# Performance work log

Measured on AMD Instinct MI355X. Metric: run time of the kernel, lower is better.

Reference implementation:

```python
import jax, jax.numpy as jnp
import numpy as np

B, D_IN, D_OUT = 8192, 4096, 2048

def setup_inputs() -> dict:
    key = jax.random.key(0)
    k1, k2, k3 = jax.random.split(key, 3)
    inputs = jax.random.normal(k1, (B, D_IN), dtype=jnp.float32)
    # xavier-uniform kernel
    limit = float(np.sqrt(6.0 / (D_IN + D_OUT)))
    kernel = jax.random.uniform(k2, (D_IN, D_OUT), dtype=jnp.float32, minval=-limit, maxval=limit)
    bias = jnp.zeros((D_OUT,), dtype=jnp.float32)
    map_ = jax.random.bernoulli(k3, p=0.1, shape=(D_IN, D_OUT)).astype(jnp.float32)
    return {"inputs": inputs, "kernel": kernel, "bias": bias, "map": map_}

def reference(inputs, kernel, bias, map):
    # SparseTF: mask the weight in place, then dense GEMM + bias
    masked_kernel = kernel * map            # [D_IN, D_OUT]
    out = inputs @ masked_kernel + bias     # [B, D_OUT]
    return out
```

## Files before the change

### kernel.cpp

```cpp
#include <hip/hip_runtime.h>

#define BB   8192
#define DIN  4096
#define DOUT 2048

typedef unsigned short ushort_t;
typedef __attribute__((ext_vector_type(8))) short bf16x8;
typedef __attribute__((ext_vector_type(4))) float f32x4;

__device__ inline ushort_t f2bf(float f) {
    union { float f; unsigned u; } v; v.f = f;
    unsigned u = v.u;
    return (ushort_t)((u + 0x7fffu + ((u >> 16) & 1u)) >> 16);
}

#define GLOAD16(g, s)                                                        \
    __builtin_amdgcn_global_load_lds(                                        \
        (const __attribute__((address_space(1))) void*)(g),                  \
        (__attribute__((address_space(3))) void*)(s), 16, 0, 0)

#define FENCE()  asm volatile("" ::: "memory")
#define BAR()    do { FENCE(); __builtin_amdgcn_s_barrier(); FENCE(); } while (0)
#define VMCNT(n) asm volatile("s_waitcnt vmcnt(" #n ")" ::: "memory")
#define LGKM(n)  asm volatile("s_waitcnt lgkmcnt(" #n ")" ::: "memory")
#define SCHB()   __builtin_amdgcn_sched_barrier(0)

struct __align__(8) us4 { ushort_t x, y, z, w; };

__global__ __launch_bounds__(256) void convA(const float4* __restrict__ in,
                                             us4* __restrict__ out, int n4) {
    int i = blockIdx.x * blockDim.x + threadIdx.x;
    int stride = gridDim.x * blockDim.x;
    for (; i < n4; i += stride) {
        float4 v = in[i];
        us4 o;
        o.x = f2bf(v.x); o.y = f2bf(v.y); o.z = f2bf(v.z); o.w = f2bf(v.w);
        out[i] = o;
    }
}

__global__ __launch_bounds__(256) void maskT(const float* __restrict__ Kn,
                                             const float* __restrict__ Mp,
                                             ushort_t* __restrict__ WT) {
    __shared__ ushort_t t[32][33];
    const int n0 = blockIdx.x * 32;
    const int k0 = blockIdx.y * 32;
    const int tx = threadIdx.x, ty = threadIdx.y;
    #pragma unroll
    for (int i = ty; i < 32; i += 8) {
        size_t idx = (size_t)(k0 + i) * DOUT + (n0 + tx);
        t[i][tx] = f2bf(Kn[idx] * Mp[idx]);
    }
    __syncthreads();
    #pragma unroll
    for (int i = ty; i < 32; i += 8) {
        WT[(size_t)(n0 + i) * DIN + (k0 + tx)] = t[tx][i];
    }
}

__global__ __launch_bounds__(512) void gemm8(const ushort_t* __restrict__ A,
                                             const ushort_t* __restrict__ BT,
                                             const float* __restrict__ bias,
                                             float* __restrict__ C) {
    constexpr int K = DIN, N = DOUT;
    constexpr int NT = K / 64;
    extern __shared__ char sb[];

    const int tid  = threadIdx.x;
    const int lane = tid & 63;
    const int w    = tid >> 6;
    const int wr   = w >> 2;
    const int wcn  = w & 3;
    const int l15  = lane & 15;

    const int orig = blockIdx.y * 8 + blockIdx.x;
    const int swz  = (orig & 7) * 32 + (orig >> 3);
    const int n0   = (swz & 7) * 256;
    const int m0   = (swz >> 3) * 256;

    const int srow = lane >> 3;
    const int scol = ((lane & 7) ^ srow) * 8;
    const ushort_t* Ag = A  + (size_t)(m0 + srow) * K + scol;
    const ushort_t* Bg = BT + (size_t)(n0 + srow) * K + scol;

    auto stgA = [&](int buf, int kt, int h, int c) {
        GLOAD16(Ag + (size_t)(h * 128 + c * 8) * K + kt * 64,
                sb + buf * 65536 + h * 16384 + c * 1024);
    };
    auto stgB = [&](int buf, int kt, int h, int c) {
        GLOAD16(Bg + (size_t)(h * 128 + c * 8) * K + kt * 64,
                sb + buf * 65536 + 32768 + h * 16384 + c * 1024);
    };
#define STAGE_TILE(BUF, KT)                                                    \
    do {                                                                       \
        stgA(BUF, KT, 0, w); stgA(BUF, KT, 0, 8 + w);                          \
        stgA(BUF, KT, 1, w); stgA(BUF, KT, 1, 8 + w);                          \
        stgB(BUF, KT, 0, w); stgB(BUF, KT, 0, 8 + w);                          \
        stgB(BUF, KT, 1, w); stgB(BUF, KT, 1, 8 + w);                          \
    } while (0)

    const int fxor = (l15 & 7) << 4;
    const int kq   = (lane >> 4) * 16;

    f32x4 acc[8][4] = {};

#define RDA(DST, MH, KS)                                                       \
    _Pragma("unroll") for (int mm = 0; mm < 4; ++mm)                           \
        DST[mm] = *(const bf16x8*)(An_ + ((MH) * 4 + mm) * 2048 + l15 * 128 +  \
                                   (((KS) * 64 + kq) ^ fxor));
#define RDB(DST, KS)                                                           \
    _Pragma("unroll") for (int nn = 0; nn < 4; ++nn)                           \
        DST[nn] = *(const bf16x8*)(Bn_ + nn * 2048 + l15 * 128 +               \
                                   (((KS) * 64 + kq) ^ fxor));
#define MCL(MH, AFS, BFS)                                                      \
    __builtin_amdgcn_s_setprio(1);                                             \
    _Pragma("unroll") for (int mm = 0; mm < 4; ++mm)                           \
        _Pragma("unroll") for (int nn = 0; nn < 4; ++nn)                       \
            acc[(MH) * 4 + mm][nn] = __builtin_amdgcn_mfma_f32_16x16x32_bf16(  \
                AFS[mm], BFS[nn], acc[(MH) * 4 + mm][nn], 0, 0, 0);            \
    __builtin_amdgcn_s_setprio(0);

    STAGE_TILE(0, 0);
    VMCNT(0);
    BAR();

    int cur = 0;
    for (int t = 0; t < NT; ++t) {
        const char* An_ = sb + cur * 65536 + wr * 16384;
        const char* Bn_ = sb + cur * 65536 + 32768 + (wcn >> 1) * 16384 +
                          (wcn & 1) * 8192;
        const bool pf = (t + 1 < NT);
        if (pf) STAGE_TILE(1 - cur, t + 1);

        bf16x8 bf0[4], bf1[4], afA[4], afB[4];
        RDB(bf0, 0); RDA(afA, 0, 0); RDA(afB, 1, 0);
        LGKM(4); SCHB();
        MCL(0, afA, bf0);
        RDB(bf1, 1); RDA(afA, 0, 1);
        LGKM(8); SCHB();
        MCL(1, afB, bf0);
        RDA(afB, 1, 1);
        LGKM(4); SCHB();
        MCL(0, afA, bf1);
        LGKM(0); SCHB();
        MCL(1, afB, bf1);
        if (pf) { VMCNT(0); }
        BAR();
        cur ^= 1;
    }
#undef MCL
#undef RDA
#undef RDB
#undef STAGE_TILE

    #pragma unroll
    for (int n = 0; n < 4; ++n) {
        const int col = n0 + wcn * 64 + n * 16 + l15;
        const float bv = bias[col];
        #pragma unroll
        for (int m = 0; m < 8; ++m) {
            const int r0 = m0 + wr * 128 + m * 16 + (lane >> 4) * 4;
            #pragma unroll
            for (int j = 0; j < 4; ++j)
                C[(size_t)(r0 + j) * N + col] = acc[m][n][j] + bv;
        }
    }
}

__global__ __launch_bounds__(1024) void gemm_fb(const float* __restrict__ A,
                                                const float* __restrict__ Kn,
                                                const float* __restrict__ Mp,
                                                const float* __restrict__ bias,
                                                float* __restrict__ C) {
    __shared__ float As[32][33];
    __shared__ float Bs[32][33];
    const int tx = threadIdx.x, ty = threadIdx.y;
    const int row = blockIdx.y * 32 + ty;
    const int col = blockIdx.x * 32 + tx;
    float acc = 0.f;
    for (int kt = 0; kt < DIN; kt += 32) {
        As[ty][tx] = A[(size_t)row * DIN + kt + tx];
        size_t bidx = (size_t)(kt + ty) * DOUT + col;
        Bs[ty][tx] = Kn[bidx] * Mp[bidx];
        __syncthreads();
        #pragma unroll
        for (int kk = 0; kk < 32; ++kk)
            acc += As[ty][kk] * Bs[kk][tx];
        __syncthreads();
    }
    C[(size_t)row * DOUT + col] = acc + bias[col];
}

extern "C" void kernel_launch(void* const* d_in, const int* in_sizes, int n_in,
                              void* d_out, int out_size, void* d_ws, size_t ws_size,
                              hipStream_t stream) {
    const float* inputs = (const float*)d_in[0];
    const float* kernel = (const float*)d_in[1];
    const float* bias   = (const float*)d_in[2];
    const float* map    = (const float*)d_in[3];
    float* out = (float*)d_out;

    const size_t abytes = (size_t)BB * DIN * sizeof(ushort_t);
    const size_t wbytes = (size_t)DIN * DOUT * sizeof(ushort_t);

    if (ws_size >= abytes + wbytes) {
        ushort_t* Abf = (ushort_t*)d_ws;
        ushort_t* WT  = (ushort_t*)((char*)d_ws + abytes);

        static bool attr_set = false;
        if (!attr_set) {
            hipFuncSetAttribute((const void*)gemm8,
                                hipFuncAttributeMaxDynamicSharedMemorySize, 131072);
            attr_set = true;
        }

        convA<<<2048, 256, 0, stream>>>((const float4*)inputs, (us4*)Abf,
                                        (int)((size_t)BB * DIN / 4));
        maskT<<<dim3(DOUT / 32, DIN / 32), dim3(32, 8), 0, stream>>>(kernel, map, WT);
        gemm8<<<dim3(DOUT / 256, BB / 256), 512, 131072, stream>>>(Abf, WT, bias, out);
    } else {
        gemm_fb<<<dim3(DOUT / 32, BB / 32), dim3(32, 32), 0, stream>>>(inputs, kernel, map,
                                                                       bias, out);
    }
}
```

Measured before the change: 164.2 us.

## Use 4-wave blocks with 32x32x16 MFMA and 128x128 per-wave tiles

New measurement: 174.4 us. +6.2%, slower.

```diff
diff --git a/kernel.cpp b/kernel.cpp
--- a/kernel.cpp
+++ b/kernel.cpp
@@ -6,7 +6,7 @@
 
 typedef unsigned short ushort_t;
 typedef __attribute__((ext_vector_type(8))) short bf16x8;
-typedef __attribute__((ext_vector_type(4))) float f32x4;
+typedef __attribute__((ext_vector_type(16))) float f32x16;
 
 __device__ inline ushort_t f2bf(float f) {
     union { float f; unsigned u; } v; v.f = f;
@@ -58,10 +58,10 @@
     }
 }
 
-__global__ __launch_bounds__(512) void gemm8(const ushort_t* __restrict__ A,
-                                             const ushort_t* __restrict__ BT,
-                                             const float* __restrict__ bias,
-                                             float* __restrict__ C) {
+__global__ __launch_bounds__(256, 1) void gemm4(const ushort_t* __restrict__ A,
+                                                const ushort_t* __restrict__ BT,
+                                                const float* __restrict__ bias,
+                                                float* __restrict__ C) {
     constexpr int K = DIN, N = DOUT;
     constexpr int NT = K / 64;
     extern __shared__ char sb[];
@@ -69,9 +69,10 @@
     const int tid  = threadIdx.x;
     const int lane = tid & 63;
     const int w    = tid >> 6;
-    const int wr   = w >> 2;
-    const int wcn  = w & 3;
-    const int l15  = lane & 15;
+    const int wr   = w >> 1;
+    const int wc   = w & 1;
+    const int l31  = lane & 31;
+    const int hi   = lane >> 5;
 
     const int orig = blockIdx.y * 8 + blockIdx.x;
     const int swz  = (orig & 7) * 32 + (orig >> 3);
@@ -93,32 +94,32 @@
     };
 #define STAGE_TILE(BUF, KT)                                                    \
     do {                                                                       \
-        stgA(BUF, KT, 0, w); stgA(BUF, KT, 0, 8 + w);                          \
-        stgA(BUF, KT, 1, w); stgA(BUF, KT, 1, 8 + w);                          \
-        stgB(BUF, KT, 0, w); stgB(BUF, KT, 0, 8 + w);                          \
-        stgB(BUF, KT, 1, w); stgB(BUF, KT, 1, 8 + w);                          \
+        stgA(BUF, KT, 0, w);      stgA(BUF, KT, 1, w);                         \
+        stgB(BUF, KT, 0, w);      stgB(BUF, KT, 1, w);                         \
+        stgA(BUF, KT, 0, 4 + w);  stgA(BUF, KT, 1, 4 + w);                     \
+        stgB(BUF, KT, 0, 4 + w);  stgB(BUF, KT, 1, 4 + w);                     \
+        stgA(BUF, KT, 0, 8 + w);  stgA(BUF, KT, 1, 8 + w);                     \
+        stgB(BUF, KT, 0, 8 + w);  stgB(BUF, KT, 1, 8 + w);                     \
+        stgA(BUF, KT, 0, 12 + w); stgA(BUF, KT, 1, 12 + w);                    \
+        stgB(BUF, KT, 0, 12 + w); stgB(BUF, KT, 1, 12 + w);                    \
     } while (0)
 
-    const int fxor = (l15 & 7) << 4;
-    const int kq   = (lane >> 4) * 16;
-
-    f32x4 acc[8][4] = {};
-
-#define RDA(DST, MH, KS)                                                       \
-    _Pragma("unroll") for (int mm = 0; mm < 4; ++mm)                           \
-        DST[mm] = *(const bf16x8*)(An_ + ((MH) * 4 + mm) * 2048 + l15 * 128 +  \
-                                   (((KS) * 64 + kq) ^ fxor));
-#define RDB(DST, KS)                                                           \
-    _Pragma("unroll") for (int nn = 0; nn < 4; ++nn)                           \
-        DST[nn] = *(const bf16x8*)(Bn_ + nn * 2048 + l15 * 128 +               \
-                                   (((KS) * 64 + kq) ^ fxor));
-#define MCL(MH, AFS, BFS)                                                      \
-    __builtin_amdgcn_s_setprio(1);                                             \
-    _Pragma("unroll") for (int mm = 0; mm < 4; ++mm)                           \
-        _Pragma("unroll") for (int nn = 0; nn < 4; ++nn)                       \
-            acc[(MH) * 4 + mm][nn] = __builtin_amdgcn_mfma_f32_16x16x32_bf16(  \
-                AFS[mm], BFS[nn], acc[(MH) * 4 + mm][nn], 0, 0, 0);            \
-    __builtin_amdgcn_s_setprio(0);
+    const int fxor = (lane & 7) << 4;
+
+#define RD(AD, BD, KS)                                                         \
+    _Pragma("unroll") for (int f = 0; f < 4; ++f) {                            \
+        AD[f] = *(const bf16x8*)(Ab_ + f * 4096 + l31 * 128 +                  \
+                                 (((((KS) << 5) | (hi << 4))) ^ fxor));        \
+        BD[f] = *(const bf16x8*)(Bb_ + f * 4096 + l31 * 128 +                  \
+                                 (((((KS) << 5) | (hi << 4))) ^ fxor));        \
+    }
+#define MCL(AS, BS)                                                            \
+    _Pragma("unroll") for (int fm = 0; fm < 4; ++fm)                           \
+        _Pragma("unroll") for (int fn = 0; fn < 4; ++fn)                       \
+            acc[fm][fn] = __builtin_amdgcn_mfma_f32_32x32x16_bf16(             \
+                AS[fm], BS[fn], acc[fm][fn], 0, 0, 0);
+
+    f32x16 acc[4][4] = {};
 
     STAGE_TILE(0, 0);
     VMCNT(0);
@@ -126,43 +127,44 @@
 
     int cur = 0;
     for (int t = 0; t < NT; ++t) {
-        const char* An_ = sb + cur * 65536 + wr * 16384;
-        const char* Bn_ = sb + cur * 65536 + 32768 + (wcn >> 1) * 16384 +
-                          (wcn & 1) * 8192;
+        const char* Ab_ = sb + cur * 65536 + wr * 16384;
+        const char* Bb_ = sb + cur * 65536 + 32768 + wc * 16384;
         const bool pf = (t + 1 < NT);
+
+        bf16x8 a0[4], b0[4], a1[4], b1[4];
+        RD(a0, b0, 0);
         if (pf) STAGE_TILE(1 - cur, t + 1);
-
-        bf16x8 bf0[4], bf1[4], afA[4], afB[4];
-        RDB(bf0, 0); RDA(afA, 0, 0); RDA(afB, 1, 0);
-        LGKM(4); SCHB();
-        MCL(0, afA, bf0);
-        RDB(bf1, 1); RDA(afA, 0, 1);
+        RD(a1, b1, 1);
         LGKM(8); SCHB();
-        MCL(1, afB, bf0);
-        RDA(afB, 1, 1);
-        LGKM(4); SCHB();
-        MCL(0, afA, bf1);
+        MCL(a0, b0);
+        RD(a0, b0, 2);
+        LGKM(8); SCHB();
+        MCL(a1, b1);
+        RD(a1, b1, 3);
+        LGKM(8); SCHB();
+        MCL(a0, b0);
         LGKM(0); SCHB();
-        MCL(1, afB, bf1);
-        if (pf) { VMCNT(0); }
+        MCL(a1, b1);
+        VMCNT(0);
         BAR();
         cur ^= 1;
     }
 #undef MCL
-#undef RDA
-#undef RDB
+#undef RD
 #undef STAGE_TILE
 
     #pragma unroll
-    for (int n = 0; n < 4; ++n) {
-        const int col = n0 + wcn * 64 + n * 16 + l15;
+    for (int fn = 0; fn < 4; ++fn) {
+        const int col = n0 + wc * 128 + fn * 32 + l31;
         const float bv = bias[col];
         #pragma unroll
-        for (int m = 0; m < 8; ++m) {
-            const int r0 = m0 + wr * 128 + m * 16 + (lane >> 4) * 4;
+        for (int fm = 0; fm < 4; ++fm) {
+            const int r0 = m0 + wr * 128 + fm * 32 + 4 * hi;
             #pragma unroll
-            for (int j = 0; j < 4; ++j)
-                C[(size_t)(r0 + j) * N + col] = acc[m][n][j] + bv;
+            for (int reg = 0; reg < 16; ++reg) {
+                const int row = r0 + (reg & 3) + 8 * (reg >> 2);
+                C[(size_t)row * N + col] = acc[fm][fn][reg] + bv;
+            }
         }
     }
 }
@@ -209,7 +211,7 @@
 
         static bool attr_set = false;
         if (!attr_set) {
-            hipFuncSetAttribute((const void*)gemm8,
+            hipFuncSetAttribute((const void*)gemm4,
                                 hipFuncAttributeMaxDynamicSharedMemorySize, 131072);
             attr_set = true;
         }
@@ -217,7 +219,7 @@
         convA<<<2048, 256, 0, stream>>>((const float4*)inputs, (us4*)Abf,
                                         (int)((size_t)BB * DIN / 4));
         maskT<<<dim3(DOUT / 32, DIN / 32), dim3(32, 8), 0, stream>>>(kernel, map, WT);
-        gemm8<<<dim3(DOUT / 256, BB / 256), 512, 131072, stream>>>(Abf, WT, bias, out);
+        gemm4<<<dim3(DOUT / 256, BB / 256), 256, 131072, stream>>>(Abf, WT, bias, out);
     } else {
         gemm_fb<<<dim3(DOUT / 32, BB / 32), dim3(32, 32), 0, stream>>>(inputs, kernel, map,
                                                                        bias, out);
```
